# Kernel tuning notes

Measured on AMD Instinct MI355X. Metric: run time of the kernel, lower is better.

## Reference

```python
import jax, jax.numpy as jnp
import numpy as np

L = 18                      # chain length -> Hilbert dim 2^L
J1 = 1.0                    # fixed exchange coupling (not trainable)
M_KRYLOV = 64               # Lanczos subspace size (>= n_eigs)
DIM = 2 ** L

# spin-1/2 operators (S = sigma/2)
SX = 0.5 * jnp.array([[0., 1.], [1., 0.]], jnp.float32)
SZ = 0.5 * jnp.array([[1., 0.], [0., -1.]], jnp.float32)
# two-site Heisenberg bond S_i.S_j in basis |00>,|01>,|10>,|11> (real: SxSx+SySy = flip terms)
BOND = jnp.array([[0.25, 0., 0., 0.],
                  [0., -0.25, 0.5, 0.],
                  [0., 0.5, -0.25, 0.],
                  [0., 0., 0., 0.25]], jnp.float32)


def setup_inputs() -> dict:
    key = jax.random.key(0)
    phi = jnp.asarray(2.0 * np.pi * np.arange(L) / L, jnp.float32)
    phi = phi + 0.01 * jax.random.normal(key, (L,), jnp.float32)
    return {
        "B_0": jnp.float32(0.2),
        "B_ext": jnp.float32(0.05),
        "phi_i": phi,
        "n_eigs": 4,
    }


def _matvec(v, field_ops):
    """Matrix-free H @ v for the open Heisenberg chain with site fields.
    v: (DIM,), field_ops: (L, 2, 2)."""
    out = jnp.zeros_like(v)
    bond = jnp.float32(J1) * BOND
    for i in range(L - 1):  # fixed structural loop over bonds
        blk = v.reshape(2 ** i, 4, 2 ** (L - i - 2))
        out = out + jnp.einsum('ab,xbz->xaz', bond, blk).reshape(-1)
    for i in range(L):      # fixed structural loop over sites (Zeeman term)
        blk = v.reshape(2 ** i, 2, 2 ** (L - i - 1))
        out = out + jnp.einsum('ab,xbz->xaz', field_ops[i], blk).reshape(-1)
    return out


def _lanczos(field_ops, v0, m):
    """m-step Lanczos; returns Krylov basis V (m, DIM) and tridiag coeffs."""
    def step(carry, _):
        v_prev, v, beta_prev = carry
        w = _matvec(v, field_ops)
        alpha = jnp.vdot(v, w)
        w = w - alpha * v - beta_prev * v_prev
        beta = jnp.sqrt(jnp.vdot(w, w))
        v_next = w / jnp.maximum(beta, jnp.float32(1e-12))
        return (v, v_next, beta), (v, alpha, beta)

    init = (jnp.zeros_like(v0), v0, jnp.float32(0.0))
    _, (V, alphas, betas) = jax.lax.scan(step, init, None, length=m)
    return V, alphas, betas


def reference(B_0, B_ext, phi_i, n_eigs):
    # skyrmion-texture field: in-plane/out-of-plane components from phi_i
    Bx = B_0 * jnp.sin(phi_i)
    Bz = B_0 * jnp.cos(phi_i) + B_ext
    field_ops = Bx[:, None, None] * SX + Bz[:, None, None] * SZ  # (L,2,2)

    v0 = jax.random.normal(jax.random.key(42), (DIM,), jnp.float32)  # v_init='randn'
    v0 = v0 / jnp.sqrt(jnp.vdot(v0, v0))

    V, a, b = _lanczos(field_ops, v0, M_KRYLOV)
    T = jnp.diag(a) + jnp.diag(b[:-1], 1) + jnp.diag(b[:-1], -1)  # (m,m) tridiag
    w, U = jnp.linalg.eigh(T)
    eigvals = w[:n_eigs]                                   # lowest n_eigs Ritz values
    eigvecs = jnp.einsum('md,mk->dk', V, U[:, :n_eigs])    # Ritz vectors (DIM, n_eigs)
    return eigvals, eigvecs
```

## Files before the change

### kernel.cpp

```cpp
#include <hip/hip_runtime.h>
#include <stdint.h>

#define L 18
#define DIM (1 << L)
#define MKRY 64
#define NBLK 256
#define TPB 1024

__device__ __forceinline__ uint32_t rotl32(uint32_t v, int r){ return (v<<r)|(v>>(32-r)); }

__device__ __forceinline__ void threefry2x32(uint32_t k0, uint32_t k1, uint32_t x0, uint32_t x1,
                                             uint32_t& o0, uint32_t& o1) {
  uint32_t k2 = k0 ^ k1 ^ 0x1BD11BDAu;
  x0 += k0; x1 += k1;
  x0+=x1; x1=rotl32(x1,13); x1^=x0;
  x0+=x1; x1=rotl32(x1,15); x1^=x0;
  x0+=x1; x1=rotl32(x1,26); x1^=x0;
  x0+=x1; x1=rotl32(x1,6);  x1^=x0;
  x0+=k1; x1+=k2+1u;
  x0+=x1; x1=rotl32(x1,17); x1^=x0;
  x0+=x1; x1=rotl32(x1,29); x1^=x0;
  x0+=x1; x1=rotl32(x1,16); x1^=x0;
  x0+=x1; x1=rotl32(x1,24); x1^=x0;
  x0+=k2; x1+=k0+2u;
  x0+=x1; x1=rotl32(x1,13); x1^=x0;
  x0+=x1; x1=rotl32(x1,15); x1^=x0;
  x0+=x1; x1=rotl32(x1,26); x1^=x0;
  x0+=x1; x1=rotl32(x1,6);  x1^=x0;
  x0+=k0; x1+=k1+3u;
  x0+=x1; x1=rotl32(x1,17); x1^=x0;
  x0+=x1; x1=rotl32(x1,29); x1^=x0;
  x0+=x1; x1=rotl32(x1,16); x1^=x0;
  x0+=x1; x1=rotl32(x1,24); x1^=x0;
  x0+=k1; x1+=k2+4u;
  x0+=x1; x1=rotl32(x1,13); x1^=x0;
  x0+=x1; x1=rotl32(x1,15); x1^=x0;
  x0+=x1; x1=rotl32(x1,26); x1^=x0;
  x0+=x1; x1=rotl32(x1,6);  x1^=x0;
  x0+=k2; x1+=k0+5u;
  o0=x0; o1=x1;
}

__device__ float jax_erfinv(float x){
  #pragma clang fp contract(off)
  float w = -log1pf(-x*x);
  float p;
  if (w < 5.0f) {
    w = w - 2.5f;
    p = 2.81022636e-08f;
    p = 3.43273939e-07f + p*w;
    p = -3.5233877e-06f + p*w;
    p = -4.39150654e-06f + p*w;
    p = 0.00021858087f + p*w;
    p = -0.00125372503f + p*w;
    p = -0.00417768164f + p*w;
    p = 0.246640727f + p*w;
    p = 1.50140941f + p*w;
  } else {
    w = sqrtf(w) - 3.0f;
    p = -0.000200214257f;
    p = 0.000100950558f + p*w;
    p = 0.00134934322f + p*w;
    p = -0.00367342844f + p*w;
    p = 0.00573950773f + p*w;
    p = -0.0076224613f + p*w;
    p = 0.00943887047f + p*w;
    p = 1.00167406f + p*w;
    p = 2.83297682f + p*w;
  }
  return p*x;
}

__device__ __forceinline__ float rng_val(unsigned i){
  #pragma clang fp contract(off)
  uint32_t o0,o1; threefry2x32(0u,42u,0u,i,o0,o1);
  uint32_t bits = o0 ^ o1;
  float f = __uint_as_float((bits >> 9) | 0x3f800000u) - 1.0f;
  const float lo = -0.99999994f;
  float u = f*2.0f;
  u = u + lo;
  u = fmaxf(lo, u);
  return 1.41421354f * jax_erfinv(u);
}

__device__ __forceinline__ double2 blockReduce2(double a, double b){
  __shared__ double sa[16], sb[16], res[2];
  int lane = threadIdx.x & 63, wid = threadIdx.x >> 6;
  #pragma unroll
  for (int off=32; off; off>>=1){ a += __shfl_down(a,off,64); b += __shfl_down(b,off,64); }
  if (lane==0){ sa[wid]=a; sb[wid]=b; }
  __syncthreads();
  if (wid==0){
    double xa = (lane<16)? sa[lane] : 0.0;
    double xb = (lane<16)? sb[lane] : 0.0;
    #pragma unroll
    for (int off=8; off; off>>=1){ xa += __shfl_down(xa,off,64); xb += __shfl_down(xb,off,64); }
    if (lane==0){ res[0]=xa; res[1]=xb; }
  }
  __syncthreads();
  double2 r; r.x=res[0]; r.y=res[1];
  return r;
}

__device__ __forceinline__ void gbar2(unsigned* bar, unsigned epoch){
  __syncthreads();
  if (threadIdx.x==0){
    const int st = (blockIdx.x & 7)*32;
    __hip_atomic_fetch_add(&bar[st], 1u, __ATOMIC_ACQ_REL, __HIP_MEMORY_SCOPE_AGENT);
    if (blockIdx.x==0){
      unsigned guard=0;
      for (;;){
        unsigned sum=0;
        #pragma unroll
        for (int k=0;k<8;++k)
          sum += __hip_atomic_load(&bar[k*32], __ATOMIC_ACQUIRE, __HIP_MEMORY_SCOPE_AGENT);
        if (sum >= (unsigned)NBLK) break;
        __builtin_amdgcn_s_sleep(1);
        if (++guard > (1u<<22)) break;
      }
      #pragma unroll
      for (int k=0;k<8;++k)
        __hip_atomic_store(&bar[k*32], 0u, __ATOMIC_RELAXED, __HIP_MEMORY_SCOPE_AGENT);
      __hip_atomic_fetch_add(&bar[256], 1u, __ATOMIC_RELEASE, __HIP_MEMORY_SCOPE_AGENT);
    } else {
      unsigned guard=0;
      while (__hip_atomic_load(&bar[256], __ATOMIC_RELAXED, __HIP_MEMORY_SCOPE_AGENT) < epoch){
        __builtin_amdgcn_s_sleep(1);
        if (++guard > (1u<<22)) break;
      }
      (void)__hip_atomic_load(&bar[256], __ATOMIC_ACQUIRE, __HIP_MEMORY_SCOPE_AGENT);
    }
  }
  __syncthreads();
}

#define CM_INIT {3u<<16,3u<<15,3u<<14,3u<<13,3u<<12,3u<<11,3u<<10,3u<<9, \
                 1u<<17,1u<<16,1u<<15,1u<<14,1u<<13,1u<<12,1u<<11,1u<<10}

__device__ __forceinline__ float matvec1(int s, int tid, float vs,
                                         const float* __restrict__ lds_v,
                                         const float2 (*__restrict__ lds_h)[TPB],
                                         const float* __restrict__ hxz){
  #pragma clang fp contract(off)
  float acc = 0.0f;
  #pragma unroll
  for (int i=0;i<L-1;++i){
    const int q = L-2-i;
    const unsigned msk = 3u<<q;
    const unsigned b2 = ((unsigned)s >> q) & 3u;
    float nbv;
    if (i<=7) nbv = lds_h[i][tid].x;
    else      nbv = lds_v[((unsigned)s ^ msk) & (TPB-1u)];
    if (b2==0u || b2==3u){ acc = acc + 0.25f*vs; }
    else if (b2==1u){ float t = -0.25f*vs; t = t + 0.5f*nbv; acc = acc + t; }
    else            { float t = 0.5f*nbv; t = t + (-0.25f)*vs; acc = acc + t; }
  }
  #pragma unroll
  for (int i=0;i<L;++i){
    const int p = L-1-i;
    const unsigned msk = 1u<<p;
    const float hx = hxz[i], hz = hxz[18+i];
    float nbv;
    if (i<=7) nbv = lds_h[8+i][tid].x;
    else      nbv = lds_v[((unsigned)s ^ msk) & (TPB-1u)];
    float t;
    if ((unsigned)s & msk){ t = hx*nbv; t = t + (-hz)*vs; }
    else                  { t = hz*vs;  t = t + hx*nbv; }
    acc = acc + t;
  }
  return acc;
}


__global__ void k_init(unsigned* bar){ int t=threadIdx.x; if (t<512) bar[t]=0u; }

__global__ void __launch_bounds__(TPB) k_pass1(const float* __restrict__ B0,
        const float* __restrict__ Bext, const float* __restrict__ phi,
        float* __restrict__ vbase, int vmod, float* __restrict__ wring,
        double* __restrict__ part, float* scal, unsigned* bar){
  __shared__ float lds_v[TPB];
  __shared__ float2 lds_h[16][TPB];
  __shared__ float lds_hxz[36];
  const unsigned CM[16] = CM_INIT;
  const int tid = threadIdx.x, bid = blockIdx.x;
  const int s = bid*TPB + tid;

  if (bid==0 && tid < L){
    #pragma clang fp contract(off)
    float b0 = B0[0], be = Bext[0];
    double ph = (double)phi[tid];
    float Bx = b0*(float)sin(ph);
    float Bz = b0*(float)cos(ph);
    Bz = Bz + be;
    scal[130+tid] = 0.5f*Bx;
    scal[148+tid] = 0.5f*Bz;
  }

  float n = rng_val((unsigned)s);
  {
    double2 pr = blockReduce2((double)n*(double)n, 0.0);
    if (tid==0){ part[512+2*bid]=pr.x; part[512+2*bid+1]=pr.y; }
  }
  gbar2(bar, 1);

  if (tid < 36) lds_hxz[tid] = scal[130+tid];

  float nrm;
  {
    double xa = (tid<NBLK)? part[512+2*tid] : 0.0;
    double xb = (tid<NBLK)? part[512+2*tid+1] : 0.0;
    double2 t = blockReduce2(xa, xb);
    nrm = (float)sqrt(t.x);
  }
  float v = __fdiv_rn(n, nrm), vp = 0.0f, b_p = 0.0f;
  vbase[s] = v;
  if (s==0) scal[129] = nrm;

  #pragma unroll
  for (int ci=0; ci<16; ++ci)
    lds_h[ci][tid] = make_float2(__fdiv_rn(rng_val((unsigned)s ^ CM[ci]), nrm), 0.0f);
  lds_v[tid] = v;
  __syncthreads();

  for (int m=0; m<MKRY; ++m){
    float w = matvec1(s, tid, v, lds_v, lds_h, lds_hxz);
    wring[(size_t)(m&1)*DIM + s] = w;

    double2 p2 = blockReduce2((double)v*(double)w, (double)w*(double)w);
    double* pb = part + (size_t)(m&1)*512;
    if (tid==0){ pb[2*bid]=p2.x; pb[2*bid+1]=p2.y; }
    gbar2(bar, 2+(unsigned)m);

    float wn[16];
    const float* wr = wring + (size_t)(m&1)*DIM;
    #pragma unroll
    for (int ci=0; ci<16; ++ci) wn[ci] = wr[(unsigned)s ^ CM[ci]];

    double xa = (tid<NBLK)? pb[2*tid] : 0.0;
    double xb = (tid<NBLK)? pb[2*tid+1] : 0.0;
    double2 tt = blockReduce2(xa, xb);
    float alpha = (float)tt.x;
    double b2d = tt.y - tt.x*tt.x - (double)b_p*(double)b_p;
    float beta = (float)sqrt(fmax(b2d, 0.0));
    float bden = fmaxf(beta, 1e-12f);

    float vn;
    {
      #pragma clang fp contract(off)
      float x = w - alpha*v;
      x = x - b_p*vp;
      vn = __fdiv_rn(x, bden);
    }
    vbase[(size_t)((m+1)%vmod)*DIM + s] = vn;

    #pragma unroll
    for (int ci=0; ci<16; ++ci){
      #pragma clang fp contract(off)
      float2 hh = lds_h[ci][tid];
      float x = wn[ci] - alpha*hh.x;
      x = x - b_p*hh.y;
      float hn = __fdiv_rn(x, bden);
      lds_h[ci][tid] = make_float2(hn, hh.x);
    }

    if (s==0){ scal[m]=alpha; scal[64+m]=beta; }
    vp=v; v=vn; b_p=beta;
    lds_v[tid]=vn;
    __syncthreads();
  }
}

__global__ void __launch_bounds__(256) k_pass2s(const float* __restrict__ vbase,
        const float* __restrict__ scal, float* __restrict__ out){
  __shared__ float U[256];
  int tid = threadIdx.x;
  int s = blockIdx.x*256 + tid;
  U[tid] = scal[192+tid];
  __syncthreads();
  {
    #pragma clang fp contract(off)
    float o0=0.0f,o1=0.0f,o2=0.0f,o3=0.0f;
    for (int m=0;m<MKRY;++m){
      float vm = vbase[(size_t)m*DIM + s];
      o0 = o0 + vm*U[4*m+0];
      o1 = o1 + vm*U[4*m+1];
      o2 = o2 + vm*U[4*m+2];
      o3 = o3 + vm*U[4*m+3];
    }
    *(float4*)(out + 4 + 4*(size_t)s) = make_float4(o0,o1,o2,o3);
  }
}

__global__ void __launch_bounds__(TPB) k_pass2c(float* __restrict__ wring,
        const float* __restrict__ scal, float* __restrict__ out, unsigned* bar){
  __shared__ float lds_v[TPB];
  __shared__ float2 lds_h[16][TPB];
  __shared__ float lds_hxz[36];
  __shared__ float lds_ab[384];
  const unsigned CM[16] = CM_INIT;
  const int tid = threadIdx.x, bid = blockIdx.x;
  const int s = bid*TPB + tid;
  if (tid < 36) lds_hxz[tid] = scal[130+tid];
  if (tid < 128) lds_ab[tid] = scal[tid];
  if (tid >= 128 && tid < 384) lds_ab[tid] = scal[192 + (tid-128)];
  const float nrm = scal[129];
  float v = __fdiv_rn(rng_val((unsigned)s), nrm), vp = 0.0f;
  #pragma unroll
  for (int ci=0; ci<16; ++ci)
    lds_h[ci][tid] = make_float2(__fdiv_rn(rng_val((unsigned)s ^ CM[ci]), nrm), 0.0f);
  lds_v[tid] = v;
  __syncthreads();
  float o0=0.0f,o1=0.0f,o2=0.0f,o3=0.0f;
  for (int m=0;m<MKRY;++m){
    float w = matvec1(s, tid, v, lds_v, lds_h, lds_hxz);
    wring[(size_t)(m&1)*DIM + s] = w;
    {
      #pragma clang fp contract(off)
      o0 = o0 + v*lds_ab[128+4*m+0];
      o1 = o1 + v*lds_ab[128+4*m+1];
      o2 = o2 + v*lds_ab[128+4*m+2];
      o3 = o3 + v*lds_ab[128+4*m+3];
    }
    gbar2(bar, 66+(unsigned)m);
    float wn[16];
    const float* wr = wring + (size_t)(m&1)*DIM;
    #pragma unroll
    for (int ci=0; ci<16; ++ci) wn[ci] = wr[(unsigned)s ^ CM[ci]];
    float alpha = lds_ab[m];
    float bp = (m==0)? 0.0f : lds_ab[64+m-1];
    float bden = fmaxf(lds_ab[64+m], 1e-12f);
    float vn;
    {
      #pragma clang fp contract(off)
      float x = w - alpha*v;
      x = x - bp*vp;
      vn = __fdiv_rn(x, bden);
    }
    #pragma unroll
    for (int ci=0; ci<16; ++ci){
      #pragma clang fp contract(off)
      float2 hh = lds_h[ci][tid];
      float x = wn[ci] - alpha*hh.x;
      x = x - bp*hh.y;
      float hn = __fdiv_rn(x, bden);
      lds_h[ci][tid] = make_float2(hn, hh.x);
    }
    vp=v; v=vn;
    lds_v[tid]=vn;
    __syncthreads();
  }
  *(float4*)(out + 4 + 4*(size_t)s) = make_float4(o0,o1,o2,o3);
}

__global__ void k_eigh(float* __restrict__ scal, float* __restrict__ out){
  __shared__ double Z[64][65];
  int t = threadIdx.x;
  double ddv = (double)scal[t];
  double eev = (t<63)? (double)scal[64+t] : 0.0;
  for (int j=0;j<64;++j) Z[t][j] = (t==j)?1.0:0.0;
  __syncthreads();

  for (int l=0;l<64;++l){
    for (int iter=0; iter<80; ++iter){
      double dt1 = __shfl_down(ddv, 1, 64);
      bool cond = (t>=l) && (t<63) &&
                  (fabs(eev) <= 2.220446049250313e-16 * (fabs(ddv)+fabs(dt1)));
      unsigned long long bm = __ballot(cond) | (1ull<<63);
      int m = (int)__builtin_ctzll(bm);
      if (m==l) break;
      double dd_l  = __shfl(ddv, l, 64);
      double dd_l1 = __shfl(ddv, l+1, 64);
      double dd_m  = __shfl(ddv, m, 64);
      double ee_l  = __shfl(eev, l, 64);
      double g = (dd_l1-dd_l)/(2.0*ee_l);
      double r = sqrt(fma(g,g,1.0));
      g = dd_m-dd_l + ee_l/(g + copysign(r,g));
      double s=1.0, c=1.0, p=0.0;
      int stop = l;
      double ee_i  = __shfl(eev, m-1, 64);
      double dd_i  = __shfl(ddv, m-1, 64);
      double dd_i1 = dd_m;
      double zhi = Z[t][m];
      for (int i=m-1; i>=l; --i){
        double ee_n=0.0, dd_n=0.0;
        if (i>l){ ee_n = __shfl(eev, i-1, 64); dd_n = __shfl(ddv, i-1, 64); }
        double f = s*ee_i, b = c*ee_i;
        double h = fma(f,f,g*g);
        if (h==0.0){
          if (t==i+1) ddv = dd_i1 - p;
          if (t==m) eev = 0.0;
          stop = i+1;
          break;
        }
        double inv;
        if (h < 1e-35){
          inv = 1.0/sqrt(h);
        } else {
          double x0 = (double)__frsqrt_rn((float)h);
          x0 = x0*(1.5 - 0.5*h*x0*x0);
          inv = x0*(1.5 - 0.5*h*x0*x0);
        }
        s = f*inv; c = g*inv;
        double rr = h*inv;
        g = dd_i1 - p;
        double r2 = (dd_i - g)*s + 2.0*c*b;
        p = s*r2;
        double ddw = g + p;
        g = c*r2 - b;
        if (t==i+1){ ddv = ddw; eev = rr; }
        double zlo = Z[t][i];
        Z[t][i+1] = s*zlo + c*zhi;
        zhi = c*zlo - s*zhi;
        dd_i1 = dd_i; ee_i = ee_n; dd_i = dd_n;
        if (i==l){
          if (t==l){ ddv = ddv - p; eev = g; }
          if (t==m){ eev = 0.0; }
        }
      }
      Z[t][stop] = zhi;
      __syncthreads();
    }
  }
  double dvm = ddv;
  #pragma unroll
  for (int k=0;k<4;++k){
    double mv = dvm; int mi = t;
    #pragma unroll
    for (int off=32; off; off>>=1){
      double ov = __shfl_down(mv, off, 64);
      int    oi = __shfl_down(mi, off, 64);
      if (ov < mv || (ov==mv && oi<mi)){ mv=ov; mi=oi; }
    }
    int jm = __shfl(mi, 0, 64);
    double lv = __shfl(mv, 0, 64);
    if (t==jm) dvm = 1.0e300;
    scal[192 + t*4 + k] = (float)Z[t][jm];
    if (t==k) out[k] = (float)lv;
  }
}

extern "C" void kernel_launch(void* const* d_in, const int* in_sizes, int n_in,
                              void* d_out, int out_size, void* d_ws, size_t ws_size,
                              hipStream_t stream){
  (void)in_sizes; (void)n_in; (void)out_size;
  const float* B0   = (const float*)d_in[0];
  const float* Bext = (const float*)d_in[1];
  const float* phi  = (const float*)d_in[2];
  float* out = (float*)d_out;

  size_t need_big = ((size_t)(MKRY+3)*DIM)*4 + 16384;
  int vmod; bool big;
  if (ws_size >= need_big) { vmod = MKRY+1; big = true; }
  else                     { vmod = 3;      big = false; }

  float* vbase = (float*)d_ws;
  float* wring = vbase + (size_t)vmod*DIM;
  double* part = (double*)(wring + 2*(size_t)DIM);
  float* scal  = (float*)(part + 1024);
  unsigned* bar = (unsigned*)(scal + 512);

  hipLaunchKernelGGL(k_init, dim3(1), dim3(512), 0, stream, bar);
  {
    void* args[] = { (void*)&B0, (void*)&Bext, (void*)&phi,
                     (void*)&vbase, (void*)&vmod, (void*)&wring,
                     (void*)&part, (void*)&scal, (void*)&bar };
    (void)hipLaunchCooperativeKernel((const void*)k_pass1, dim3(NBLK), dim3(TPB), args, 0, stream);
  }
  hipLaunchKernelGGL(k_eigh, dim3(1), dim3(64), 0, stream, scal, out);
  if (big){
    hipLaunchKernelGGL(k_pass2s, dim3(DIM/256), dim3(256), 0, stream, vbase, scal, out);
  } else {
    void* args[] = { (void*)&wring, (void*)&scal, (void*)&out, (void*)&bar };
    (void)hipLaunchCooperativeKernel((const void*)k_pass2c, dim3(NBLK), dim3(TPB), args, 0, stream);
  }
}
```

Measured before the change: 2.574 ms.

## Have block 0 reduce Lanczos scalars and broadcast them through the grid barrier

The old full grid barrier, after which every block re-reduced all 256 partial sums, is split. Block 0 now waits for all arrivals, reduces the partials, writes alpha, beta or the norm to global memory and releases an epoch flag. The other blocks spin on that flag and read the scalars back. This removes the redundant 256-block reduction, at the cost of serialising the release behind block 0's reduction. The eigensolver's double Newton step for the reciprocal square root is also cut to a single refinement, which may lose precision.

```diff
diff --git a/kernel.cpp b/kernel.cpp
--- a/kernel.cpp
+++ b/kernel.cpp
@@ -134,6 +134,26 @@
   __syncthreads();
 }
 
+__device__ __forceinline__ void gbar_arrive_spin0(unsigned* bar){
+  const int st = (blockIdx.x & 7)*32;
+  __hip_atomic_fetch_add(&bar[st], 1u, __ATOMIC_ACQ_REL, __HIP_MEMORY_SCOPE_AGENT);
+  if (blockIdx.x==0){
+    unsigned guard=0;
+    for (;;){
+      unsigned sum=0;
+      #pragma unroll
+      for (int k=0;k<8;++k)
+        sum += __hip_atomic_load(&bar[k*32], __ATOMIC_ACQUIRE, __HIP_MEMORY_SCOPE_AGENT);
+      if (sum >= (unsigned)NBLK) break;
+      __builtin_amdgcn_s_sleep(1);
+      if (++guard > (1u<<22)) break;
+    }
+    #pragma unroll
+    for (int k=0;k<8;++k)
+      __hip_atomic_store(&bar[k*32], 0u, __ATOMIC_RELAXED, __HIP_MEMORY_SCOPE_AGENT);
+  }
+}
+
 #define CM_INIT {3u<<16,3u<<15,3u<<14,3u<<13,3u<<12,3u<<11,3u<<10,3u<<9, \
                  1u<<17,1u<<16,1u<<15,1u<<14,1u<<13,1u<<12,1u<<11,1u<<10}
 
@@ -201,20 +221,35 @@
     double2 pr = blockReduce2((double)n*(double)n, 0.0);
     if (tid==0){ part[512+2*bid]=pr.x; part[512+2*bid+1]=pr.y; }
   }
-  gbar2(bar, 1);
-
-  if (tid < 36) lds_hxz[tid] = scal[130+tid];
-
   float nrm;
-  {
+  if (tid==0) gbar_arrive_spin0(bar);
+  if (bid==0){
+    __syncthreads();
     double xa = (tid<NBLK)? part[512+2*tid] : 0.0;
     double xb = (tid<NBLK)? part[512+2*tid+1] : 0.0;
-    double2 t = blockReduce2(xa, xb);
-    nrm = (float)sqrt(t.x);
-  }
+    double2 t2 = blockReduce2(xa, xb);
+    nrm = (float)sqrt(t2.x);
+    if (tid==0){
+      scal[129] = nrm;
+      __hip_atomic_fetch_add(&bar[256], 1u, __ATOMIC_RELEASE, __HIP_MEMORY_SCOPE_AGENT);
+    }
+  } else {
+    if (tid==0){
+      unsigned guard=0;
+      while (__hip_atomic_load(&bar[256], __ATOMIC_RELAXED, __HIP_MEMORY_SCOPE_AGENT) < 1u){
+        __builtin_amdgcn_s_sleep(1);
+        if (++guard > (1u<<22)) break;
+      }
+      (void)__hip_atomic_load(&bar[256], __ATOMIC_ACQUIRE, __HIP_MEMORY_SCOPE_AGENT);
+    }
+    __syncthreads();
+    nrm = scal[129];
+  }
+
+  if (tid < 36) lds_hxz[tid] = scal[130+tid];
+
   float v = __fdiv_rn(n, nrm), vp = 0.0f, b_p = 0.0f;
   vbase[s] = v;
-  if (s==0) scal[129] = nrm;
 
   #pragma unroll
   for (int ci=0; ci<16; ++ci)
@@ -229,20 +264,40 @@
     double2 p2 = blockReduce2((double)v*(double)w, (double)w*(double)w);
     double* pb = part + (size_t)(m&1)*512;
     if (tid==0){ pb[2*bid]=p2.x; pb[2*bid+1]=p2.y; }
-    gbar2(bar, 2+(unsigned)m);
+
+    float alpha, beta;
+    if (tid==0) gbar_arrive_spin0(bar);
+    if (bid==0){
+      __syncthreads();
+      double xa = (tid<NBLK)? pb[2*tid] : 0.0;
+      double xb = (tid<NBLK)? pb[2*tid+1] : 0.0;
+      double2 tt = blockReduce2(xa, xb);
+      alpha = (float)tt.x;
+      double b2d = tt.y - tt.x*tt.x - (double)b_p*(double)b_p;
+      beta = (float)sqrt(fmax(b2d, 0.0));
+      if (tid==0){
+        scal[m] = alpha; scal[64+m] = beta;
+        __hip_atomic_fetch_add(&bar[256], 1u, __ATOMIC_RELEASE, __HIP_MEMORY_SCOPE_AGENT);
+      }
+    } else {
+      if (tid==0){
+        unsigned guard=0;
+        unsigned ep = 2u + (unsigned)m;
+        while (__hip_atomic_load(&bar[256], __ATOMIC_RELAXED, __HIP_MEMORY_SCOPE_AGENT) < ep){
+          __builtin_amdgcn_s_sleep(1);
+          if (++guard > (1u<<22)) break;
+        }
+        (void)__hip_atomic_load(&bar[256], __ATOMIC_ACQUIRE, __HIP_MEMORY_SCOPE_AGENT);
+      }
+      __syncthreads();
+      alpha = scal[m]; beta = scal[64+m];
+    }
+    float bden = fmaxf(beta, 1e-12f);
 
     float wn[16];
     const float* wr = wring + (size_t)(m&1)*DIM;
     #pragma unroll
     for (int ci=0; ci<16; ++ci) wn[ci] = wr[(unsigned)s ^ CM[ci]];
-
-    double xa = (tid<NBLK)? pb[2*tid] : 0.0;
-    double xb = (tid<NBLK)? pb[2*tid+1] : 0.0;
-    double2 tt = blockReduce2(xa, xb);
-    float alpha = (float)tt.x;
-    double b2d = tt.y - tt.x*tt.x - (double)b_p*(double)b_p;
-    float beta = (float)sqrt(fmax(b2d, 0.0));
-    float bden = fmaxf(beta, 1e-12f);
 
     float vn;
     {
@@ -263,7 +318,6 @@
       lds_h[ci][tid] = make_float2(hn, hh.x);
     }
 
-    if (s==0){ scal[m]=alpha; scal[64+m]=beta; }
     vp=v; v=vn; b_p=beta;
     lds_v[tid]=vn;
     __syncthreads();
@@ -397,8 +451,7 @@
           inv = 1.0/sqrt(h);
         } else {
           double x0 = (double)__frsqrt_rn((float)h);
-          x0 = x0*(1.5 - 0.5*h*x0*x0);
-          inv = x0*(1.5 - 0.5*h*x0*x0);
+          inv = x0*(1.5 - (0.5*h)*(x0*x0));
         }
         s = f*inv; c = g*inv;
         double rr = h*inv;
```

After: 2.420 ms. -6.0%, faster.
